# Kernel tuning notes

Hardware: AMD Instinct MI355X
Metric: run time of the kernel (lower is better)

The kernel has to match this reference:

```python
import jax, jax.numpy as jnp
import numpy as np

HEIGHT = 32
SIGMA = 2.0
NUM_NEGATIVE = 4096
N, C = 32, 512
L = HEIGHT * HEIGHT


def _grid_weight(height: int, sigma: float) -> jnp.ndarray:
    # distance_weights: pairwise Euclidean distance between grid points
    ii, jj = np.meshgrid(np.arange(height), np.arange(height), indexing='ij')
    coords = np.stack([ii.ravel(), jj.ravel()], axis=1).astype(np.float32)  # [L, 2]
    d2 = ((coords[:, None, :] - coords[None, :, :]) ** 2).sum(-1)  # squared dist [L, L]
    w = -(0.5 / sigma ** 2) * d2
    np.fill_diagonal(w, -np.inf)
    return jax.nn.softmax(jnp.asarray(w, dtype=jnp.float32), axis=1)


def setup_inputs() -> dict:
    key = jax.random.key(0)
    k1, k2 = jax.random.split(key)
    embedding = jax.random.normal(k1, (N, L, C), dtype=jnp.float32)
    weight = _grid_weight(HEIGHT, SIGMA)  # [L, L] softmax-normalized grid kernel
    neg_indices = jax.random.randint(k2, (NUM_NEGATIVE,), 0, N * L, dtype=jnp.int64)
    return {"embedding": embedding, "weight": weight, "neg_indices": neg_indices}


def reference(embedding, weight, neg_indices):
    n, l, c = embedding.shape
    # F.normalize(dim=-1), eps=1e-12
    norm = jnp.maximum(jnp.linalg.norm(embedding, axis=-1, keepdims=True), 1e-12)
    e = embedding / norm  # [N, L, C]
    # target = weight @ e  (broadcast over batch)
    target = jnp.einsum('kl,nlc->nkc', weight, e)  # [N, L, C]
    sim_pos = jnp.sum(e * target, axis=-1)  # [N, L]
    flat = e.reshape(-1, c)  # [N*L, C]
    negatives = flat[neg_indices]  # [M, C]
    sim_neg = jnp.einsum('nlc,mc->nlm', e, negatives)  # [N, L, M]
    logits = jnp.concatenate([sim_pos[..., None], sim_neg], axis=2).reshape(n * l, 1 + neg_indices.shape[0])
    # CrossEntropyLoss with target class 0, mean reduction
    loss = -jnp.mean(jax.nn.log_softmax(logits, axis=-1)[:, 0])
    return loss
```

## Files before the change

### kernel.cpp

```cpp
#include <hip/hip_runtime.h>
#include <hip/hip_bf16.h>
#include <stdint.h>

#define L_DIM 1024
#define C_DIM 512
#define CB4 256
#define N_BATCH 32
#define M_NEG 4096
#define NROWS (N_BATCH * L_DIM)

typedef float f32x4 __attribute__((ext_vector_type(4)));
typedef int i32x4 __attribute__((ext_vector_type(4)));
typedef int i32x8 __attribute__((ext_vector_type(8)));

#define E4_SCALE 32.0f
#define MX_SCALE 122
#define FMT_FP4 4

__device__ __forceinline__ void gl_lds16(const uint8_t* g, uint8_t* l) {
  __builtin_amdgcn_global_load_lds(
      (const __attribute__((address_space(1))) void*)g,
      (__attribute__((address_space(3))) void*)l, 16, 0, 0);
}

__device__ __forceinline__ uint32_t fp4_enc(float x) {
  const uint32_t s = (__float_as_uint(x) >> 31) << 3;
  const float a = fabsf(x);
  uint32_t c;
  c = a < 0.25f ? 0u
    : a < 0.75f ? 1u
    : a < 1.25f ? 2u
    : a < 1.75f ? 3u
    : a < 2.5f  ? 4u
    : a < 3.5f  ? 5u
    : a < 5.0f  ? 6u : 7u;
  return s | c;
}

__device__ __forceinline__ i32x8 fp4_op(i32x4 d) {
  return __builtin_shufflevector(d, d, 0, 1, 2, 3, -1, -1, -1, -1);
}

__global__ __launch_bounds__(256) void k_normalize(const float* __restrict__ emb,
                                                   uint8_t* __restrict__ out,
                                                   float* __restrict__ zerobuf,
                                                   float* __restrict__ loss_out) {
  if (blockIdx.x < 256) zerobuf[blockIdx.x * 256 + threadIdx.x] = 0.0f;
  if (blockIdx.x == 0 && threadIdx.x == 0) loss_out[0] = 0.0f;
  const int lane = threadIdx.x & 63;
  const int wave = threadIdx.x >> 6;
  const long row = (long)blockIdx.x * 4 + wave;
  const float4* src = (const float4*)(emb + row * C_DIM);
  float4 v0 = src[2 * lane];
  float4 v1 = src[2 * lane + 1];
  float ss = v0.x * v0.x + v0.y * v0.y + v0.z * v0.z + v0.w * v0.w +
             v1.x * v1.x + v1.y * v1.y + v1.z * v1.z + v1.w * v1.w;
#pragma unroll
  for (int off = 1; off < 64; off <<= 1) ss += __shfl_xor(ss, off, 64);
  const float s = E4_SCALE / fmaxf(sqrtf(ss), 1e-12f);
  uint32_t pk = fp4_enc(v0.x * s)        | (fp4_enc(v0.y * s) << 4) |
                (fp4_enc(v0.z * s) << 8) | (fp4_enc(v0.w * s) << 12) |
                (fp4_enc(v1.x * s) << 16)| (fp4_enc(v1.y * s) << 20) |
                (fp4_enc(v1.z * s) << 24)| (fp4_enc(v1.w * s) << 28);
  ((uint32_t*)(out + row * CB4))[lane] = pk;
}

__global__ __launch_bounds__(256, 2) void k_gemm_fused(
    const uint8_t* __restrict__ E4, const int* __restrict__ idx,
    const float* __restrict__ W, float* __restrict__ rowsum,
    float* __restrict__ simpos) {
  __shared__ __align__(16) unsigned char smem_raw[65536];
  uint8_t* sA = (uint8_t*)smem_raw;
  uint8_t* sB = sA + 128 * 256;

  const int tid = threadIdx.x;
  const int lane = tid & 63;
  const int wave = tid >> 6;
  const int wm = wave >> 1, wn = wave & 1;
  const int q = lane >> 4, c16 = lane & 15;

  const int bid = blockIdx.x;
  const bool is0 = bid >= 2048;
  long rowBase, colBase, n = 0;
  if (is0) {
    const int t = bid - 2048;
    const int xcd = t & 7, slot = t >> 3;
    rowBase = (long)(xcd * 32 + (slot & 31)) * 128;
    colBase = (long)(slot >> 5) * 128;
  } else {
    const int xcd = bid & 7, slot = bid >> 3;
    n = xcd * 4 + (slot & 3);
    const int inner = slot >> 2;
    rowBase = (long)(inner & 7) * 128;
    colBase = (long)(inner >> 3) * 128;
  }
  const long aBase = is0 ? rowBase : n * L_DIM + rowBase;

  long offB[8];
#pragma unroll
  for (int r = 0; r < 8; ++r) {
    const int c = r * 256 + tid;
    const int rw = c >> 4, cb = c & 15;
    const long bRow = is0 ? (long)idx[colBase + rw] : n * L_DIM + colBase + rw;
    offB[r] = bRow * CB4 + (cb ^ (rw & 15)) * 16;
  }
  long offA[8];
#pragma unroll
  for (int r = 0; r < 8; ++r) {
    const int c = r * 256 + tid;
    const int rw = c >> 4, cb = c & 15;
    offA[r] = (aBase + rw) * CB4 + (cb ^ (rw & 15)) * 16;
  }

#pragma unroll
  for (int r = 0; r < 8; ++r)
    gl_lds16(E4 + offB[r], sB + (r * 256 + tid) * 16);
#pragma unroll
  for (int r = 0; r < 8; ++r)
    gl_lds16(E4 + offA[r], sA + (r * 256 + tid) * 16);
  __syncthreads();

  f32x4 acc[4][4] = {};

#pragma unroll
  for (int ks = 0; ks < 4; ++ks) {
    const int ksl = ks * 4 + q;
    i32x8 bfr[4];
#pragma unroll
    for (int j = 0; j < 4; ++j) {
      const int row = wn * 64 + j * 16 + c16;
      bfr[j] =
          fp4_op(*(const i32x4*)(sB + row * 256 + ((ksl ^ (row & 15)) * 16)));
    }
#pragma unroll
    for (int i = 0; i < 4; ++i) {
      const int row = wm * 64 + i * 16 + c16;
      i32x8 af =
          fp4_op(*(const i32x4*)(sA + row * 256 + ((ksl ^ (row & 15)) * 16)));
#pragma unroll
      for (int j = 0; j < 4; ++j)
        acc[i][j] = __builtin_amdgcn_mfma_scale_f32_16x16x128_f8f6f4(
            af, bfr[j], acc[i][j], FMT_FP4, FMT_FP4,
            0, MX_SCALE, 0, MX_SCALE);
    }
  }
  __syncthreads();

  if (is0) {
    float* S = (float*)smem_raw;
#pragma unroll
    for (int i = 0; i < 4; ++i)
#pragma unroll
      for (int r = 0; r < 4; ++r) {
        const float s = __expf(acc[i][0][r]) + __expf(acc[i][1][r]) +
                        __expf(acc[i][2][r]) + __expf(acc[i][3][r]);
        S[wave * 1280 + (i * 16 + q * 4 + r) * 20 + c16] = s;
      }
    __syncthreads();
    if (tid < 128) {
      const int wmr = tid >> 6, row64 = tid & 63;
      const float* p0 = S + (wmr * 2 + 0) * 1280 + row64 * 20;
      const float* p1 = S + (wmr * 2 + 1) * 1280 + row64 * 20;
      float4 t0 = ((const float4*)p0)[0], t1 = ((const float4*)p0)[1];
      float4 t2 = ((const float4*)p0)[2], t3 = ((const float4*)p0)[3];
      float4 u0 = ((const float4*)p1)[0], u1 = ((const float4*)p1)[1];
      float4 u2 = ((const float4*)p1)[2], u3 = ((const float4*)p1)[3];
      float v = t0.x + t0.y + t0.z + t0.w + t1.x + t1.y + t1.z + t1.w +
                t2.x + t2.y + t2.z + t2.w + t3.x + t3.y + t3.z + t3.w +
                u0.x + u0.y + u0.z + u0.w + u1.x + u1.y + u1.z + u1.w +
                u2.x + u2.y + u2.z + u2.w + u3.x + u3.y + u3.z + u3.w;
      atomicAdd(&rowsum[rowBase + tid], v);
    }
  } else {
    float* G = (float*)smem_raw;
#pragma unroll
    for (int p = 0; p < 2; ++p) {
      if (wm == p) {
#pragma unroll
        for (int i = 0; i < 4; ++i)
#pragma unroll
          for (int j = 0; j < 4; ++j)
#pragma unroll
            for (int r = 0; r < 4; ++r)
              G[(i * 16 + q * 4 + r) * 132 + wn * 64 + j * 16 + c16] =
                  acc[i][j][r];
      }
      __syncthreads();
      {
        const int rr = tid >> 2;
        const int chunk = tid & 3;
        const long krow = rowBase + p * 64 + rr;
        float v = 0.0f;
#pragma unroll
        for (int u = 0; u < 8; ++u) {
          const float4 g = *(const float4*)(G + rr * 132 + u * 16 + chunk * 4);
          const float4 w4 =
              *(const float4*)(W + krow * L_DIM + colBase + u * 16 + chunk * 4);
          v += g.x * w4.x + g.y * w4.y + g.z * w4.z + g.w * w4.w;
        }
        v += __shfl_xor(v, 1, 64);
        v += __shfl_xor(v, 2, 64);
        if (chunk == 0) atomicAdd(&simpos[n * L_DIM + krow], v);
      }
      __syncthreads();
    }
  }
}

__global__ __launch_bounds__(256) void k_finalize(const float* __restrict__ rowsum,
                                                  const float* __restrict__ simpos,
                                                  float* __restrict__ out) {
  const int gid = blockIdx.x * 256 + threadIdx.x;
  const float sp = simpos[gid];
  float v = __logf(rowsum[gid] + __expf(sp)) - sp;
#pragma unroll
  for (int off = 1; off < 64; off <<= 1) v += __shfl_xor(v, off, 64);
  __shared__ float ws[4];
  if ((threadIdx.x & 63) == 0) ws[threadIdx.x >> 6] = v;
  __syncthreads();
  if (threadIdx.x == 0)
    atomicAdd(out, (ws[0] + ws[1] + ws[2] + ws[3]) * (1.0f / (float)NROWS));
}

extern "C" void kernel_launch(void* const* d_in, const int* in_sizes, int n_in,
                              void* d_out, int out_size, void* d_ws, size_t ws_size,
                              hipStream_t stream) {
  const float* emb = (const float*)d_in[0];
  const float* weight = (const float*)d_in[1];
  const int* negidx = (const int*)d_in[2];
  float* out = (float*)d_out;
  char* ws = (char*)d_ws;

  uint8_t* E4 = (uint8_t*)ws;
  float* rowsum = (float*)(ws + 8388608);
  float* simpos = (float*)(ws + 8519680);

  k_normalize<<<NROWS / 4, 256, 0, stream>>>(emb, E4, rowsum, out);
  k_gemm_fused<<<10240, 256, 0, stream>>>(E4, negidx, weight, rowsum, simpos);
  k_finalize<<<NROWS / 256, 256, 0, stream>>>(rowsum, simpos, out);
}
```

Measured before the change: 189.0 us.

## Stream K-dimension in 64-byte chunks to shrink LDS and raise occupancy

```diff
diff --git a/kernel.cpp b/kernel.cpp
--- a/kernel.cpp
+++ b/kernel.cpp
@@ -17,10 +17,11 @@
 #define MX_SCALE 122
 #define FMT_FP4 4
 
+template <int GOFF>
 __device__ __forceinline__ void gl_lds16(const uint8_t* g, uint8_t* l) {
   __builtin_amdgcn_global_load_lds(
       (const __attribute__((address_space(1))) void*)g,
-      (__attribute__((address_space(3))) void*)l, 16, 0, 0);
+      (__attribute__((address_space(3))) void*)l, 16, GOFF, 0);
 }
 
 __device__ __forceinline__ uint32_t fp4_enc(float x) {
@@ -65,13 +66,13 @@
   ((uint32_t*)(out + row * CB4))[lane] = pk;
 }
 
-__global__ __launch_bounds__(256, 2) void k_gemm_fused(
+__global__ __launch_bounds__(256, 4) void k_gemm_fused(
     const uint8_t* __restrict__ E4, const int* __restrict__ idx,
     const float* __restrict__ W, float* __restrict__ rowsum,
     float* __restrict__ simpos) {
-  __shared__ __align__(16) unsigned char smem_raw[65536];
+  __shared__ __align__(16) unsigned char smem_raw[20480];
   uint8_t* sA = (uint8_t*)smem_raw;
-  uint8_t* sB = sA + 128 * 256;
+  uint8_t* sB = sA + 128 * 64;
 
   const int tid = threadIdx.x;
   const int lane = tid & 63;
@@ -96,55 +97,66 @@
   }
   const long aBase = is0 ? rowBase : n * L_DIM + rowBase;
 
-  long offB[8];
-#pragma unroll
-  for (int r = 0; r < 8; ++r) {
+  const uint8_t* pA[2];
+  const uint8_t* pB[2];
+#pragma unroll
+  for (int r = 0; r < 2; ++r) {
     const int c = r * 256 + tid;
-    const int rw = c >> 4, cb = c & 15;
+    const int rw = c >> 2, cb = c & 3;
+    pA[r] = E4 + (aBase + rw) * CB4 + (cb ^ (rw & 3)) * 16;
     const long bRow = is0 ? (long)idx[colBase + rw] : n * L_DIM + colBase + rw;
-    offB[r] = bRow * CB4 + (cb ^ (rw & 15)) * 16;
-  }
-  long offA[8];
-#pragma unroll
-  for (int r = 0; r < 8; ++r) {
-    const int c = r * 256 + tid;
-    const int rw = c >> 4, cb = c & 15;
-    offA[r] = (aBase + rw) * CB4 + (cb ^ (rw & 15)) * 16;
-  }
-
-#pragma unroll
-  for (int r = 0; r < 8; ++r)
-    gl_lds16(E4 + offB[r], sB + (r * 256 + tid) * 16);
-#pragma unroll
-  for (int r = 0; r < 8; ++r)
-    gl_lds16(E4 + offA[r], sA + (r * 256 + tid) * 16);
-  __syncthreads();
+    pB[r] = E4 + bRow * CB4 + (cb ^ (rw & 3)) * 16;
+  }
+
+  int ldsB[4], ldsA[4];
+#pragma unroll
+  for (int j = 0; j < 4; ++j) {
+    const int rowB = wn * 64 + j * 16 + c16;
+    ldsB[j] = rowB * 64 + (q ^ (rowB & 3)) * 16;
+    const int rowA = wm * 64 + j * 16 + c16;
+    ldsA[j] = rowA * 64 + (q ^ (rowA & 3)) * 16;
+  }
 
   f32x4 acc[4][4] = {};
 
-#pragma unroll
-  for (int ks = 0; ks < 4; ++ks) {
-    const int ksl = ks * 4 + q;
+  auto kstep = [&](int parity) {
+    __syncthreads();
     i32x8 bfr[4];
 #pragma unroll
-    for (int j = 0; j < 4; ++j) {
-      const int row = wn * 64 + j * 16 + c16;
-      bfr[j] =
-          fp4_op(*(const i32x4*)(sB + row * 256 + ((ksl ^ (row & 15)) * 16)));
-    }
+    for (int j = 0; j < 4; ++j)
+      bfr[j] = fp4_op(*(const i32x4*)(sB + ldsB[j]));
 #pragma unroll
     for (int i = 0; i < 4; ++i) {
-      const int row = wm * 64 + i * 16 + c16;
-      i32x8 af =
-          fp4_op(*(const i32x4*)(sA + row * 256 + ((ksl ^ (row & 15)) * 16)));
+      i32x8 af = fp4_op(*(const i32x4*)(sA + ldsA[i]));
 #pragma unroll
       for (int j = 0; j < 4; ++j)
         acc[i][j] = __builtin_amdgcn_mfma_scale_f32_16x16x128_f8f6f4(
             af, bfr[j], acc[i][j], FMT_FP4, FMT_FP4,
             0, MX_SCALE, 0, MX_SCALE);
     }
-  }
-  __syncthreads();
+    __syncthreads();
+  };
+
+  gl_lds16<0>(pA[0], sA + tid * 16);
+  gl_lds16<0>(pA[1], sA + (256 + tid) * 16);
+  gl_lds16<0>(pB[0], sB + tid * 16);
+  gl_lds16<0>(pB[1], sB + (256 + tid) * 16);
+  kstep(0);
+  gl_lds16<64>(pA[0], sA + tid * 16);
+  gl_lds16<64>(pA[1], sA + (256 + tid) * 16);
+  gl_lds16<64>(pB[0], sB + tid * 16);
+  gl_lds16<64>(pB[1], sB + (256 + tid) * 16);
+  kstep(1);
+  gl_lds16<128>(pA[0], sA + tid * 16);
+  gl_lds16<128>(pA[1], sA + (256 + tid) * 16);
+  gl_lds16<128>(pB[0], sB + tid * 16);
+  gl_lds16<128>(pB[1], sB + (256 + tid) * 16);
+  kstep(2);
+  gl_lds16<192>(pA[0], sA + tid * 16);
+  gl_lds16<192>(pA[1], sA + (256 + tid) * 16);
+  gl_lds16<192>(pB[0], sB + tid * 16);
+  gl_lds16<192>(pB[1], sB + (256 + tid) * 16);
+  kstep(3);
 
   if (is0) {
     float* S = (float*)smem_raw;
@@ -158,9 +170,9 @@
       }
     __syncthreads();
     if (tid < 128) {
-      const int wmr = tid >> 6, row64 = tid & 63;
-      const float* p0 = S + (wmr * 2 + 0) * 1280 + row64 * 20;
-      const float* p1 = S + (wmr * 2 + 1) * 1280 + row64 * 20;
+      const int wm2 = tid >> 6, row64 = tid & 63;
+      const float* p0 = (const float*)S + (wm2 * 2 + 0) * 1280 + row64 * 20;
+      const float* p1 = (const float*)S + (wm2 * 2 + 1) * 1280 + row64 * 20;
       float4 t0 = ((const float4*)p0)[0], t1 = ((const float4*)p0)[1];
       float4 t2 = ((const float4*)p0)[2], t3 = ((const float4*)p0)[3];
       float4 u0 = ((const float4*)p1)[0], u1 = ((const float4*)p1)[1];
@@ -174,32 +186,36 @@
   } else {
     float* G = (float*)smem_raw;
 #pragma unroll
-    for (int p = 0; p < 2; ++p) {
-      if (wm == p) {
-#pragma unroll
-        for (int i = 0; i < 4; ++i)
+    for (int p = 0; p < 4; ++p) {
+      if (wm == (p >> 1)) {
+#pragma unroll
+        for (int ii = 0; ii < 2; ++ii) {
+          const int i = (p & 1) * 2 + ii;
 #pragma unroll
           for (int j = 0; j < 4; ++j)
 #pragma unroll
             for (int r = 0; r < 4; ++r)
-              G[(i * 16 + q * 4 + r) * 132 + wn * 64 + j * 16 + c16] =
+              G[(ii * 16 + q * 4 + r) * 132 + wn * 64 + j * 16 + c16] =
                   acc[i][j][r];
+        }
       }
       __syncthreads();
       {
-        const int rr = tid >> 2;
-        const int chunk = tid & 3;
-        const long krow = rowBase + p * 64 + rr;
+        const int rr = tid >> 3;
+        const int chunk = tid & 7;
+        const long krow = rowBase + p * 32 + rr;
         float v = 0.0f;
 #pragma unroll
-        for (int u = 0; u < 8; ++u) {
-          const float4 g = *(const float4*)(G + rr * 132 + u * 16 + chunk * 4);
-          const float4 w4 =
-              *(const float4*)(W + krow * L_DIM + colBase + u * 16 + chunk * 4);
+        for (int u = 0; u < 4; ++u) {
+          const float4 g =
+              *(const float4*)(G + rr * 132 + chunk * 16 + u * 4);
+          const float4 w4 = *(const float4*)(W + krow * L_DIM + colBase +
+                                             chunk * 16 + u * 4);
           v += g.x * w4.x + g.y * w4.y + g.z * w4.z + g.w * w4.w;
         }
         v += __shfl_xor(v, 1, 64);
         v += __shfl_xor(v, 2, 64);
+        v += __shfl_xor(v, 4, 64);
         if (chunk == 0) atomicAdd(&simpos[n * L_DIM + krow], v);
       }
       __syncthreads();
```

Measured after the change: 165.9 us. 12.2% less time.
